# Performance work log

Hardware: AMD Instinct MI355X
Metric: run time of the kernel (lower is better)

The kernel has to match this reference:

```python
import jax, jax.numpy as jnp
import numpy as np

B, T, D, V, U = 16, 1000, 512, 5000, 64


def _safe_logaddexp(a, b):
    # logaddexp with nan-safe gradients when both args are -inf
    both = jnp.isneginf(a) & jnp.isneginf(b)
    a_ = jnp.where(both, 0.0, a)
    b_ = jnp.where(both, 0.0, b)
    return jnp.where(both, -jnp.inf, jnp.logaddexp(a_, b_))


def _log_sub_exp(a, b):
    # faithful port of log_substraction_exp: log(exp(a) - exp(b)), stable
    mask1 = (~jnp.isinf(a)) & (~jnp.isinf(b))
    a_ = jnp.where(mask1, a, -1.0)
    b_ = jnp.where(mask1, b, -2.0)
    ans_tmp = b_ + jnp.log(jnp.exp(a_ - b_) - 1.0)
    a_ = jnp.where(jnp.isinf(ans_tmp), -2000.0, a_)
    b_ = jnp.where(jnp.isinf(ans_tmp), -2001.0, b_)
    ans1 = b_ + jnp.log(jnp.exp(a_ - b_) - 1.0)
    ans = jnp.where(mask1, ans1, -jnp.inf)
    mask2 = (~jnp.isinf(a)) & jnp.isinf(b)
    return jnp.where(mask2, a, ans)


def _ctc_trellis(logp, ys):
    # Standard CTC lattice over extended labels (blank interleaved), S = 2U+1.
    # alpha[t,b,s]: logprob of paths over frames 0..t ending in state s (incl. emission at t)
    # beta[t,b,s]:  logprob of emitting frames t+1..T-1 and finishing, given state s at t
    # This reproduces the k2 lattice forward/backward scores at the label states.
    Bb, Tt, _ = logp.shape
    Uu = ys.shape[1]
    S = 2 * Uu + 1
    l_ext = jnp.zeros((Bb, S), ys.dtype).at[:, 1::2].set(ys)  # blank=0 at even s
    lp = jnp.take_along_axis(logp, jnp.broadcast_to(l_ext[:, None, :], (Bb, Tt, S)), axis=2)
    skip_ok = jnp.zeros((Bb, S), bool).at[:, 3::2].set(ys[:, 1:] != ys[:, :-1])
    lpT = jnp.transpose(lp, (1, 0, 2))  # [T,B,S]
    ninf1 = jnp.full((Bb, 1), -jnp.inf)
    ninf2 = jnp.full((Bb, 2), -jnp.inf)

    a0 = jnp.full((Bb, S), -jnp.inf).at[:, :2].set(lpT[0, :, :2])

    def astep(ap, lp_t):
        s1 = jnp.concatenate([ninf1, ap[:, :-1]], 1)
        s2 = jnp.concatenate([ninf2, ap[:, :-2]], 1)
        a = lp_t + _safe_logaddexp(_safe_logaddexp(ap, s1), jnp.where(skip_ok, s2, -jnp.inf))
        return a, a

    _, arest = jax.lax.scan(astep, a0, lpT[1:])
    alpha = jnp.concatenate([a0[None], arest], 0)  # [T,B,S]

    bl = jnp.full((Bb, S), -jnp.inf).at[:, S - 2:].set(0.0)  # final states: last label / last blank
    skipL2 = jnp.concatenate([skip_ok[:, 2:], jnp.zeros((Bb, 2), bool)], 1)

    def bstep(bn, lp_next):
        m = lp_next + bn
        m1 = jnp.concatenate([m[:, 1:], ninf1], 1)
        m2 = jnp.concatenate([m[:, 2:], ninf2], 1)
        bcur = _safe_logaddexp(_safe_logaddexp(m, m1), jnp.where(skipL2, m2, -jnp.inf))
        return bcur, bcur

    _, brest = jax.lax.scan(bstep, bl, lpT[1:], reverse=True)
    beta = jnp.concatenate([brest, bl[None]], 0)  # [T,B,S]
    return alpha, beta, lp


def setup_inputs() -> dict:
    key = jax.random.key(0)
    k1, k2, k3 = jax.random.split(key, 3)
    hs_pad = jax.random.normal(k1, (B, T, D), jnp.float32)
    hlens = jnp.full((B,), T, jnp.int32)
    ys_pad = jax.random.randint(k2, (B, U), 1, V)  # labels in [1, V); 0 is blank
    ali = jnp.zeros((B, U), jnp.int32)  # unused when risk_factor == 0
    W = jax.random.normal(k3, (D, V), jnp.float32) * 0.02
    b = jnp.zeros((V,), jnp.float32)
    return {"hs_pad": hs_pad, "hlens": hlens, "ys_pad": ys_pad, "ali": ali, "W": W, "b": b}


def reference(hs_pad, hlens, ys_pad, ali, W, b):
    # ctc_lo + log_softmax (dropout_rate=0). hlens are all equal -> sort/unsort is identity.
    logp = jax.nn.log_softmax(hs_pad @ W + b, axis=-1)  # [B,T,V]
    alpha_f, beta_f, lp = _ctc_trellis(logp, ys_pad)
    alpha = jnp.transpose(alpha_f[:, :, 1::2], (1, 2, 0))  # [B,U,T]
    beta = jnp.transpose(beta_f[:, :, 1::2], (1, 2, 0))    # [B,U,T]
    p = jnp.transpose(lp[:, :, 1::2], (0, 2, 1))           # [B,U,T] logprob of label u at frame t
    # beta', excluding re-emission of label u at t+1 -> paths whose label-u segment ends at t
    bp = _log_sub_exp(beta[:, :, :-1], beta[:, :, 1:] + p[:, :, 1:])
    bp = jnp.concatenate([bp, beta[:, :, -1:]], -1)
    loss_state = alpha + bp
    loss_state = jnp.where(jnp.isnan(loss_state), -jnp.inf, loss_state)
    loss_u = jax.nn.logsumexp(loss_state, axis=2)  # aggregate == 'time'
    mask = jnp.isinf(loss_u)
    denom = (~mask).astype(loss_u.dtype).sum(1)
    loss_fsas = jnp.where(mask, 0.0, loss_u).sum(1) / denom
    Uu = ys_pad.shape[1]
    loss_fsas = jnp.where(hlens < Uu, 0.0, loss_fsas)
    return (-loss_fsas).mean()
```

## Files before the change

### kernel.cpp

```cpp
#include <hip/hip_runtime.h>

#define NB 16
#define NT 1000
#define ND 512
#define NV 5000
#define NVP 5120
#define NU 64
#define NLL 72
#define NM (NB * NT)
#define NCH 40

typedef short short8v __attribute__((ext_vector_type(8)));
typedef float float4v __attribute__((ext_vector_type(4)));

#define NEGINF (-__builtin_inff())
#define SENTL  (-1.0e30f)
#define LOG2E 1.4426950408889634f
#define LN2F  0.6931471805599453f
#define SENT2 (-2000.4586751f * LOG2E)

__device__ __forceinline__ float fexp2(float x) { return __builtin_amdgcn_exp2f(x); }
__device__ __forceinline__ float flog2(float x) { return __builtin_amdgcn_logf(x); }

__device__ __forceinline__ float dpp_shr1(float x) {
  int xi = __builtin_bit_cast(int, x);
  int r = __builtin_amdgcn_update_dpp(xi, xi, 0x138, 0xf, 0xf, false);
  return __builtin_bit_cast(float, r);
}
__device__ __forceinline__ float dpp_shl1(float x) {
  int xi = __builtin_bit_cast(int, x);
  int r = __builtin_amdgcn_update_dpp(xi, xi, 0x130, 0xf, 0xf, false);
  return __builtin_bit_cast(float, r);
}

__device__ __forceinline__ short f2bf(float x) {
  unsigned int u = __builtin_bit_cast(unsigned int, x);
  unsigned int r = (u + 0x7fffu + ((u >> 16) & 1u)) >> 16;
  return (short)(unsigned short)r;
}
__device__ __forceinline__ float bf2f(short h) {
  unsigned int u = ((unsigned int)(unsigned short)h) << 16;
  return __builtin_bit_cast(float, u);
}

__device__ __forceinline__ void g2lds16(const short* g, short* l) {
  __builtin_amdgcn_global_load_lds(
      (const __attribute__((address_space(1))) void*)g,
      (__attribute__((address_space(3))) void*)l, 16, 0, 0);
}

__device__ __forceinline__ float lae2s(float a, float b) {
  float m = fmaxf(a, b);
  return m + flog2(fexp2(a - m) + fexp2(b - m));
}
__device__ __forceinline__ float lae3s(float a, float b, float c) {
  float m = fmaxf(fmaxf(a, b), c);
  return m + flog2(fexp2(a - m) + fexp2(b - m) + fexp2(c - m));
}
__device__ __forceinline__ float lsub2(float a, float b) {
  float tmp = b + flog2(fexp2(a - b) - 1.0f);
  if (__builtin_isinf(tmp)) tmp = SENT2;
  return tmp;
}

__global__ void k_zero(float* out) {
  if (threadIdx.x == 0) out[0] = 0.0f;
}

__global__ __launch_bounds__(256) void k_cvt_hs(const float* __restrict__ in,
                                                short* __restrict__ out) {
  size_t i = (size_t)blockIdx.x * 256 + threadIdx.x;
  const float4* p = (const float4*)in + i * 2;
  float4 v0 = p[0], v1 = p[1];
  short8v r;
  r[0] = f2bf(v0.x); r[1] = f2bf(v0.y); r[2] = f2bf(v0.z); r[3] = f2bf(v0.w);
  r[4] = f2bf(v1.x); r[5] = f2bf(v1.y); r[6] = f2bf(v1.z); r[7] = f2bf(v1.w);
  int row = (int)(i >> 6);
  int g = (int)(i & 63);
  int gs = (g & ~7) | ((g & 7) ^ (row & 7));
  *(short8v*)(out + (size_t)row * ND + gs * 8) = r;
}

__global__ __launch_bounds__(256) void k_cvt_wt(const float* __restrict__ W,
                                                short* __restrict__ WT,
                                                short* __restrict__ WTlo) {
  __shared__ short tileH[64 * 72];
  __shared__ short tileL[64 * 72];
  int n0 = blockIdx.x * 64, k0 = blockIdx.y * 64;
  int tid = threadIdx.x;
  int kr = tid >> 2, part = tid & 3;
  const float* src = W + (size_t)(k0 + kr) * NV + n0 + part * 16;
#pragma unroll
  for (int jj = 0; jj < 4; ++jj) {
    int c = n0 + part * 16 + jj * 4;
    float4 v;
    if (c + 3 < NV) {
      v = *(const float4*)(src + jj * 4);
    } else {
      v.x = (c + 0 < NV) ? src[jj * 4 + 0] : 0.f;
      v.y = (c + 1 < NV) ? src[jj * 4 + 1] : 0.f;
      v.z = (c + 2 < NV) ? src[jj * 4 + 2] : 0.f;
      v.w = (c + 3 < NV) ? src[jj * 4 + 3] : 0.f;
    }
    int base = kr * 72 + part * 16 + jj * 4;
    float vv[4] = {v.x, v.y, v.z, v.w};
#pragma unroll
    for (int q = 0; q < 4; ++q) {
      short h = f2bf(vv[q]);
      tileH[base + q] = h;
      tileL[base + q] = f2bf(vv[q] - bf2f(h));
    }
  }
  __syncthreads();
  int n = tid & 63, kq = tid >> 6;
  int nn = n0 + n;
  if (nn < NVP) {
#pragma unroll
    for (int half = 0; half < 2; ++half) {
      short8v vh, vl;
#pragma unroll
      for (int jj = 0; jj < 8; ++jj) {
        vh[jj] = tileH[(kq * 16 + half * 8 + jj) * 72 + n];
        vl[jj] = tileL[(kq * 16 + half * 8 + jj) * 72 + n];
      }
      int g = (k0 >> 3) + kq * 2 + half;
      int gs = (g & ~7) | ((g & 7) ^ (nn & 7));
      *(short8v*)(WT + (size_t)nn * ND + gs * 8) = vh;
      *(short8v*)(WTlo + (size_t)nn * ND + gs * 8) = vl;
    }
  }
}

__global__ __launch_bounds__(64) void k_gather2(const short* __restrict__ WT,
                                                const short* __restrict__ WTlo,
                                                const int* __restrict__ ys,
                                                short* __restrict__ Wg_hi,
                                                short* __restrict__ Wg_lo) {
  int u = blockIdx.x, b = blockIdx.y, t = threadIdx.x;
  short8v hi = {0,0,0,0,0,0,0,0}, lo = {0,0,0,0,0,0,0,0};
  if (u < NU + 1) {
    int lab = (u == 0) ? 0 : ys[b * NU + u - 1];
    int ps = (t & ~7) | ((t & 7) ^ (lab & 7));
    hi = *(const short8v*)(WT + (size_t)lab * ND + ps * 8);
    lo = *(const short8v*)(WTlo + (size_t)lab * ND + ps * 8);
  }
  int q = (t & ~7) | ((t & 7) ^ (u & 7));
  size_t base = ((size_t)(b * 128 + u)) * ND + q * 8;
  *(short8v*)(Wg_hi + base) = hi;
  *(short8v*)(Wg_lo + base) = lo;
}

__global__ __launch_bounds__(256) void k_labg(const short* __restrict__ hsb,
                                              const short* __restrict__ Wg_hi,
                                              const short* __restrict__ Wg_lo,
                                              const int* __restrict__ ys,
                                              const float* __restrict__ bias,
                                              float* __restrict__ ll) {
  __shared__ short As[128 * 64];
  __shared__ short Bh[128 * 64];
  __shared__ short Bl[128 * 64];

  int mt = blockIdx.x, b = blockIdx.y;
  int t0 = mt * 128;
  int tid = threadIdx.x;
  int lane = tid & 63, wave = tid >> 6;
  int wm = wave >> 1, wn = wave & 1;
  int lrow = lane & 15, lkhi = lane >> 4;

  const short* gaBase = hsb + (size_t)(b * NT + t0 + wave * 32 + (lane >> 3)) * ND + (lane & 7) * 8;
  const short* ghBase = Wg_hi + (size_t)(b * 128 + wave * 32 + (lane >> 3)) * ND + (lane & 7) * 8;
  const short* glBase = Wg_lo + (size_t)(b * 128 + wave * 32 + (lane >> 3)) * ND + (lane & 7) * 8;

  float4v acc[4][4];
#pragma unroll
  for (int m = 0; m < 4; ++m)
#pragma unroll
    for (int n = 0; n < 4; ++n)
#pragma unroll
      for (int j = 0; j < 4; ++j) acc[m][n][j] = 0.f;

  for (int s = 0; s < 8; ++s) {
    int k0 = s * 64;
#pragma unroll
    for (int i = 0; i < 4; ++i) {
      g2lds16(gaBase + (size_t)(i * 8) * ND + k0, &As[(wave * 32 + i * 8) * 64]);
      g2lds16(ghBase + (size_t)(i * 8) * ND + k0, &Bh[(wave * 32 + i * 8) * 64]);
      g2lds16(glBase + (size_t)(i * 8) * ND + k0, &Bl[(wave * 32 + i * 8) * 64]);
    }
    __syncthreads();
#pragma unroll
    for (int kk = 0; kk < 2; ++kk) {
      short8v av[4], bhv[4], blv2[4];
#pragma unroll
      for (int m = 0; m < 4; ++m) {
        int r = wm * 64 + m * 16 + lrow;
        int col = (kk * 32 + lkhi * 8) ^ ((r & 7) << 3);
        av[m] = *(const short8v*)&As[r * 64 + col];
      }
#pragma unroll
      for (int n = 0; n < 4; ++n) {
        int r = wn * 64 + n * 16 + lrow;
        int col = (kk * 32 + lkhi * 8) ^ ((r & 7) << 3);
        bhv[n] = *(const short8v*)&Bh[r * 64 + col];
        blv2[n] = *(const short8v*)&Bl[r * 64 + col];
      }
#pragma unroll
      for (int m = 0; m < 4; ++m)
#pragma unroll
        for (int n = 0; n < 4; ++n) {
          acc[m][n] = __builtin_amdgcn_mfma_f32_16x16x32_bf16(av[m], bhv[n], acc[m][n], 0, 0, 0);
          acc[m][n] = __builtin_amdgcn_mfma_f32_16x16x32_bf16(av[m], blv2[n], acc[m][n], 0, 0, 0);
        }
    }
    __syncthreads();
  }

  float bu[4]; bool uval[4];
#pragma unroll
  for (int n = 0; n < 4; ++n) {
    int u = wn * 64 + n * 16 + lrow;
    uval[n] = u < NU + 1;
    int lab = (u == 0) ? 0 : (uval[n] ? ys[b * NU + u - 1] : 0);
    bu[n] = uval[n] ? bias[lab] : 0.f;
  }
#pragma unroll
  for (int m = 0; m < 4; ++m)
#pragma unroll
    for (int j = 0; j < 4; ++j) {
      int trow = t0 + wm * 64 + m * 16 + lkhi * 4 + j;
      if (trow < NT) {
#pragma unroll
        for (int n = 0; n < 4; ++n) {
          int u = wn * 64 + n * 16 + lrow;
          if (uval[n])
            ll[((size_t)(b * NLL + u)) * NT + trow] = acc[m][n][j] + bu[n];
        }
      }
    }
}

__global__ __launch_bounds__(256) void k_denom(const short* __restrict__ hsb,
                                               const short* __restrict__ WT,
                                               const float* __restrict__ bias,
                                               float* __restrict__ pm,
                                               float* __restrict__ ps) {
  __shared__ short As[128 * 64];
  __shared__ short Ws[128 * 64];
  __shared__ float mred[128][2];
  __shared__ float sred[128][2];

  int lin = blockIdx.x;
  int o = (lin & 7) * 625 + (lin >> 3);
  int mt, chunk;
  if (o < 4800) {
    int sb = o / 320, w = o % 320;
    mt = sb * 8 + (w & 7);
    chunk = w >> 3;
  } else {
    int w = o - 4800;
    mt = 120 + (w % 5);
    chunk = w / 5;
  }
  int t0 = mt * 128;
  int n0 = chunk * 128;
  int tid = threadIdx.x;
  int lane = tid & 63, wave = tid >> 6;
  int wm = wave >> 1, wn = wave & 1;
  int lrow = lane & 15, lkhi = lane >> 4;

  const short* gaBase = hsb + (size_t)(t0 + wave * 32 + (lane >> 3)) * ND + (lane & 7) * 8;
  const short* gwBase = WT + (size_t)(n0 + wave * 32 + (lane >> 3)) * ND + (lane & 7) * 8;

  float4v acc[4][4];
#pragma unroll
  for (int m = 0; m < 4; ++m)
#pragma unroll
    for (int n = 0; n < 4; ++n)
#pragma unroll
      for (int j = 0; j < 4; ++j) acc[m][n][j] = 0.f;

  auto stage = [&](int s) {
    int k0 = s * 64;
#pragma unroll
    for (int i = 0; i < 4; ++i) {
      g2lds16(gaBase + (size_t)(i * 8) * ND + k0, &As[(wave * 32 + i * 8) * 64]);
      g2lds16(gwBase + (size_t)(i * 8) * ND + k0, &Ws[(wave * 32 + i * 8) * 64]);
    }
  };
  auto compute = [&]() {
#pragma unroll
    for (int kk = 0; kk < 2; ++kk) {
      short8v av[4], wv[4];
#pragma unroll
      for (int m = 0; m < 4; ++m) {
        int r = wm * 64 + m * 16 + lrow;
        int col = (kk * 32 + lkhi * 8) ^ ((r & 7) << 3);
        av[m] = *(const short8v*)&As[r * 64 + col];
      }
#pragma unroll
      for (int n = 0; n < 4; ++n) {
        int r = wn * 64 + n * 16 + lrow;
        int col = (kk * 32 + lkhi * 8) ^ ((r & 7) << 3);
        wv[n] = *(const short8v*)&Ws[r * 64 + col];
      }
#pragma unroll
      for (int m = 0; m < 4; ++m)
#pragma unroll
        for (int n = 0; n < 4; ++n)
          acc[m][n] = __builtin_amdgcn_mfma_f32_16x16x32_bf16(av[m], wv[n], acc[m][n], 0, 0, 0);
    }
  };

  for (int s = 0; s < 8; ++s) {
    stage(s);
    __syncthreads();
    compute();
    __syncthreads();
  }

  float bcol[4]; bool cval[4];
#pragma unroll
  for (int n = 0; n < 4; ++n) {
    int c = n0 + wn * 64 + n * 16 + lrow;
    cval[n] = c < NV;
    bcol[n] = cval[n] ? bias[c] : 0.f;
  }
#pragma unroll
  for (int m = 0; m < 4; ++m)
#pragma unroll
    for (int j = 0; j < 4; ++j) {
      float mx = NEGINF;
#pragma unroll
      for (int n = 0; n < 4; ++n) {
        float v = cval[n] ? acc[m][n][j] + bcol[n] : NEGINF;
        mx = fmaxf(mx, v);
      }
#pragma unroll
      for (int d = 1; d < 16; d <<= 1) mx = fmaxf(mx, __shfl_xor(mx, d));
      float mxc = fmaxf(mx, -3.0e38f);
      float p = 0.f;
#pragma unroll
      for (int n = 0; n < 4; ++n) {
        float v = cval[n] ? acc[m][n][j] + bcol[n] : NEGINF;
        p += __expf(v - mxc);
      }
#pragma unroll
      for (int d = 1; d < 16; d <<= 1) p += __shfl_xor(p, d);
      if (lrow == 0) {
        int rloc = wm * 64 + m * 16 + lkhi * 4 + j;
        mred[rloc][wn] = mx;
        sred[rloc][wn] = p;
      }
    }
  __syncthreads();
  if (tid < 128) {
    int row = t0 + tid;
    float m0 = mred[tid][0], m1 = mred[tid][1];
    float m = fmaxf(m0, m1);
    float ss = 0.f;
    if (m != NEGINF)
      ss = ((m0 == NEGINF) ? 0.f : sred[tid][0] * __expf(m0 - m))
         + ((m1 == NEGINF) ? 0.f : sred[tid][1] * __expf(m1 - m));
    pm[(size_t)chunk * NM + row] = m;
    ps[(size_t)chunk * NM + row] = ss;
  }
}

__global__ __launch_bounds__(256) void k_dred(const float* __restrict__ pm,
                                              const float* __restrict__ ps,
                                              float* __restrict__ denom) {
  int row = blockIdx.x * 256 + threadIdx.x;
  if (row >= NM) return;
  float m = NEGINF, s = 0.f;
  for (int c = 0; c < NCH; ++c) {
    float mc = pm[(size_t)c * NM + row];
    float sc = ps[(size_t)c * NM + row];
    if (mc == NEGINF) continue;
    if (mc > m) { s = s * __expf(m - mc) + sc; m = mc; }
    else        { s += sc * __expf(mc - m); }
  }
  denom[row] = m + __logf(s);
}

__global__ __launch_bounds__(64) void k_fwdbwd(const float* __restrict__ ll,
                                               const float* __restrict__ denom,
                                               const int* __restrict__ ys,
                                               float* __restrict__ aod,
                                               float* __restrict__ bp) {
  __shared__ float denS[NT];
  __shared__ float blkS[NT];
  int bid = blockIdx.x;
  int l = threadIdx.x;
  int b = (bid < NB) ? bid : bid - NB;
  const float* llb = ll + (size_t)b * NLL * NT;
  const float* denb = denom + b * NT;
#pragma unroll
  for (int i = 0; i < 16; ++i) {
    int idx = i * 64 + l;
    if (idx < NT) { denS[idx] = denb[idx]; blkS[idx] = llb[idx]; }
  }
  __syncthreads();
  const float* lrow = llb + (size_t)(1 + l) * NT;

  if (bid < NB) {
    int lab = ys[b * NU + l];
    int labp = ys[b * NU + ((l >= 1) ? (l - 1) : 0)];
    bool skip = (l >= 1) && (lab != labp);
    float* aodb = aod + (size_t)b * NT * NU;

    float den = denS[0];
    float ae = (l == 0) ? (blkS[0] - den) * LOG2E : SENTL;
    float ao = (l == 0) ? (lrow[0] - den) * LOG2E : SENTL;
    aodb[l] = ao;

    float cl[16];
#pragma unroll
    for (int j = 0; j < 16; ++j) {
      int tt = 1 + j; if (tt > NT - 1) tt = NT - 1;
      cl[j] = lrow[tt];
    }
    for (int g = 0; g < 63; ++g) {
      float nl[16];
      if (g < 62) {
#pragma unroll
        for (int j = 0; j < 16; ++j) {
          int tt = 17 + g * 16 + j; if (tt > NT - 1) tt = NT - 1;
          nl[j] = lrow[tt];
        }
      } else {
#pragma unroll
        for (int j = 0; j < 16; ++j) nl[j] = 0.f;
      }
#pragma unroll
      for (int j = 0; j < 16; ++j) {
        int t = 1 + g * 16 + j;
        if (t < NT) {
          float d2 = denS[t];
          float pb = (blkS[t] - d2) * LOG2E, pl = (cl[j] - d2) * LOG2E;
          float po = dpp_shr1(ao); if (l == 0) po = SENTL;
          float aen = pb + lae2s(ae, po);
          float aon = pl + lae3s(ao, ae, skip ? po : SENTL);
          ae = aen; ao = aon;
          aodb[t * NU + l] = ao;
        }
      }
#pragma unroll
      for (int j = 0; j < 16; ++j) cl[j] = nl[j];
    }
  } else {
    int lab = ys[b * NU + l];
    int labn = ys[b * NU + ((l < NU - 1) ? (l + 1) : l)];
    bool skipn = (l < NU - 1) && (labn != lab);
    float* bpb = bp + (size_t)b * NT * NU;

    float bo = (l == NU - 1) ? 0.0f : SENTL;
    float be = SENTL;
    float b128 = 0.0f;
    bpb[(NT - 1) * NU + l] = bo;

    float blv[16];
#pragma unroll
    for (int j = 0; j < 16; ++j) {
      int tt = NT - 2 - j; if (tt < 0) tt = 0;
      blv[j] = lrow[tt + 1];
    }
    for (int g = 0; g < 63; ++g) {
      float nl2[16];
      if (g < 62) {
#pragma unroll
        for (int j = 0; j < 16; ++j) {
          int tt = NT - 2 - 16 * (g + 1) - j; if (tt < 0) tt = 0;
          nl2[j] = lrow[tt + 1];
        }
      } else {
#pragma unroll
        for (int j = 0; j < 16; ++j) nl2[j] = 0.f;
      }
#pragma unroll
      for (int j = 0; j < 16; ++j) {
        int t = NT - 2 - 16 * g - j;
        if (t >= 0) {
          float d2 = denS[t + 1];
          float pbv = (blkS[t + 1] - d2) * LOG2E, plv = (blv[j] - d2) * LOG2E;
          float me = pbv + be;
          float mo = plv + bo;
          float m128 = pbv + b128;
          float ne = dpp_shl1(me); if (l == NU - 1) ne = m128;
          float no = dpp_shl1(mo); if (l == NU - 1) no = SENTL;
          float ben = lae2s(me, mo);
          float bon = lae3s(mo, ne, skipn ? no : SENTL);
          bpb[t * NU + l] = lsub2(bon, mo);
          be = ben; bo = bon; b128 = m128;
        }
      }
#pragma unroll
      for (int j = 0; j < 16; ++j) blv[j] = nl2[j];
    }
  }
}

__global__ __launch_bounds__(512) void k_loss(const float* __restrict__ aod,
                                              const float* __restrict__ bp,
                                              const int* __restrict__ hlens,
                                              float* __restrict__ out) {
  __shared__ float ms[8][64], ss[8][64];
  int b = blockIdx.x, tid = threadIdx.x;
  int w = tid >> 6, l = tid & 63;
  const float* ab = aod + (size_t)b * NT * NU;
  const float* pb = bp + (size_t)b * NT * NU;
  float m = NEGINF, s = 0.f;
  int t0 = w * 125, t1 = t0 + 125;
  for (int t = t0; t < t1; ++t) {
    float x = ab[t * NU + l] + pb[t * NU + l];
    if (__builtin_isnan(x) || x < -1.0e29f) continue;
    if (x > m) { s = s * fexp2(m - x) + 1.0f; m = x; }
    else       { s += fexp2(x - m); }
  }
  ms[w][l] = m; ss[w][l] = s;
  __syncthreads();
  if (w == 0) {
    float mm = NEGINF;
#pragma unroll
    for (int i = 0; i < 8; ++i) mm = fmaxf(mm, ms[i][l]);
    float lu;
    if (mm == NEGINF) lu = NEGINF;
    else {
      float st = 0.f;
#pragma unroll
      for (int i = 0; i < 8; ++i)
        st += (ms[i][l] == NEGINF) ? 0.f : ss[i][l] * fexp2(ms[i][l] - mm);
      lu = (mm + flog2(st)) * LN2F;
    }
    bool msk = __builtin_isinf(lu);
    float sv = msk ? 0.f : lu;
    float cv = msk ? 0.f : 1.f;
#pragma unroll
    for (int d = 1; d < 64; d <<= 1) { sv += __shfl_xor(sv, d); cv += __shfl_xor(cv, d); }
    if (l == 0) {
      float lf = sv / cv;
      if (hlens[b] < NU) lf = 0.f;
      atomicAdd(out, -lf * (1.0f / NB));
    }
  }
}

extern "C" void kernel_launch(void* const* d_in, const int* in_sizes, int n_in,
                              void* d_out, int out_size, void* d_ws, size_t ws_size,
                              hipStream_t stream) {
  const float* hs    = (const float*)d_in[0];
  const int*   hlens = (const int*)d_in[1];
  const int*   ys    = (const int*)d_in[2];
  const float* W     = (const float*)d_in[4];
  const float* bias  = (const float*)d_in[5];
  float* out = (float*)d_out;

  char* ws = (char*)d_ws;
  short* hsb   = (short*)(ws + 0);
  short* WT    = (short*)(ws + 16384000);
  short* WTlo  = (short*)(ws + 21626880);
  float* pm    = (float*)(ws + 26869760);
  float* psv   = (float*)(ws + 29429760);
  float* dnm   = (float*)(ws + 31989760);
  float* ll    = (float*)(ws + 32053760);
  short* Wg_hi = (short*)(ws + 26869760);
  short* Wg_lo = (short*)(ws + 28966912);
  float* aod   = (float*)(ws + 0);
  float* bpb   = (float*)(ws + 4096000);

  k_zero<<<1, 64, 0, stream>>>(out);
  k_cvt_hs<<<4000, 256, 0, stream>>>(hs, hsb);
  k_cvt_wt<<<dim3(80, 8), 256, 0, stream>>>(W, WT, WTlo);
  k_denom<<<5000, 256, 0, stream>>>(hsb, WT, bias, pm, psv);
  k_dred<<<63, 256, 0, stream>>>(pm, psv, dnm);
  k_gather2<<<dim3(128, 16), 64, 0, stream>>>(WT, WTlo, ys, Wg_hi, Wg_lo);
  k_labg<<<dim3(8, 16), 256, 0, stream>>>(hsb, Wg_hi, Wg_lo, ys, bias, ll);
  k_fwdbwd<<<32, 64, 0, stream>>>(ll, dnm, ys, aod, bpb);
  k_loss<<<16, 512, 0, stream>>>(aod, bpb, hlens, out);
}
```

Baseline: 365.6 us.

## Overlap CTC forward pass with denominator GEMM and fold normalizer into loss

The forward alpha recursion no longer needs the softmax denominator. It runs on unnormalized label logits inside the big denominator GEMM launch, as 16 extra blocks, so the serial recursion overlaps the GEMM. The per-frame log-normalizer is recomputed from per-chunk partials in the backward kernel, and its prefix sum is subtracted from alpha in the loss kernel. The zero, conversion and reduction kernels are merged, fewer padded label rows are gathered, and lsub2 gains an early exit. This removes several launches and the serial forward pass from the critical path, at the cost of redundant reductions and a risk of precision loss from large prefix sums.

```diff
diff --git a/kernel.cpp b/kernel.cpp
--- a/kernel.cpp
+++ b/kernel.cpp
@@ -6,7 +6,8 @@
 #define NV 5000
 #define NVP 5120
 #define NU 64
-#define NLL 72
+#define NLL 66
+#define NWG 72
 #define NM (NB * NT)
 #define NCH 40
 
@@ -58,35 +59,36 @@
   return m + flog2(fexp2(a - m) + fexp2(b - m) + fexp2(c - m));
 }
 __device__ __forceinline__ float lsub2(float a, float b) {
+  if (b < -1.0e29f) return (a < -1.0e29f) ? SENTL : a;
   float tmp = b + flog2(fexp2(a - b) - 1.0f);
   if (__builtin_isinf(tmp)) tmp = SENT2;
   return tmp;
 }
 
-__global__ void k_zero(float* out) {
-  if (threadIdx.x == 0) out[0] = 0.0f;
-}
-
-__global__ __launch_bounds__(256) void k_cvt_hs(const float* __restrict__ in,
-                                                short* __restrict__ out) {
-  size_t i = (size_t)blockIdx.x * 256 + threadIdx.x;
-  const float4* p = (const float4*)in + i * 2;
-  float4 v0 = p[0], v1 = p[1];
-  short8v r;
-  r[0] = f2bf(v0.x); r[1] = f2bf(v0.y); r[2] = f2bf(v0.z); r[3] = f2bf(v0.w);
-  r[4] = f2bf(v1.x); r[5] = f2bf(v1.y); r[6] = f2bf(v1.z); r[7] = f2bf(v1.w);
-  int row = (int)(i >> 6);
-  int g = (int)(i & 63);
-  int gs = (g & ~7) | ((g & 7) ^ (row & 7));
-  *(short8v*)(out + (size_t)row * ND + gs * 8) = r;
-}
-
-__global__ __launch_bounds__(256) void k_cvt_wt(const float* __restrict__ W,
-                                                short* __restrict__ WT,
-                                                short* __restrict__ WTlo) {
+__global__ __launch_bounds__(256) void k_cvt(const float* __restrict__ hs,
+                                             const float* __restrict__ W,
+                                             short* __restrict__ hsb,
+                                             short* __restrict__ WT,
+                                             short* __restrict__ WTlo,
+                                             float* __restrict__ outv) {
   __shared__ short tileH[64 * 72];
   __shared__ short tileL[64 * 72];
-  int n0 = blockIdx.x * 64, k0 = blockIdx.y * 64;
+  if (blockIdx.x < 4000) {
+    if (blockIdx.x == 0 && threadIdx.x == 0) outv[0] = 0.0f;
+    size_t i = (size_t)blockIdx.x * 256 + threadIdx.x;
+    const float4* p = (const float4*)hs + i * 2;
+    float4 v0 = p[0], v1 = p[1];
+    short8v r;
+    r[0] = f2bf(v0.x); r[1] = f2bf(v0.y); r[2] = f2bf(v0.z); r[3] = f2bf(v0.w);
+    r[4] = f2bf(v1.x); r[5] = f2bf(v1.y); r[6] = f2bf(v1.z); r[7] = f2bf(v1.w);
+    int row = (int)(i >> 6);
+    int g = (int)(i & 63);
+    int gs = (g & ~7) | ((g & 7) ^ (row & 7));
+    *(short8v*)(hsb + (size_t)row * ND + gs * 8) = r;
+    return;
+  }
+  int bx = blockIdx.x - 4000;
+  int n0 = (bx % 80) * 64, k0 = (bx / 80) * 64;
   int tid = threadIdx.x;
   int kr = tid >> 2, part = tid & 3;
   const float* src = W + (size_t)(k0 + kr) * NV + n0 + part * 16;
@@ -145,7 +147,7 @@
     lo = *(const short8v*)(WTlo + (size_t)lab * ND + ps * 8);
   }
   int q = (t & ~7) | ((t & 7) ^ (u & 7));
-  size_t base = ((size_t)(b * 128 + u)) * ND + q * 8;
+  size_t base = ((size_t)(b * NWG + u)) * ND + q * 8;
   *(short8v*)(Wg_hi + base) = hi;
   *(short8v*)(Wg_lo + base) = lo;
 }
@@ -168,8 +170,6 @@
   int lrow = lane & 15, lkhi = lane >> 4;
 
   const short* gaBase = hsb + (size_t)(b * NT + t0 + wave * 32 + (lane >> 3)) * ND + (lane & 7) * 8;
-  const short* ghBase = Wg_hi + (size_t)(b * 128 + wave * 32 + (lane >> 3)) * ND + (lane & 7) * 8;
-  const short* glBase = Wg_lo + (size_t)(b * 128 + wave * 32 + (lane >> 3)) * ND + (lane & 7) * 8;
 
   float4v acc[4][4];
 #pragma unroll
@@ -184,8 +184,12 @@
 #pragma unroll
     for (int i = 0; i < 4; ++i) {
       g2lds16(gaBase + (size_t)(i * 8) * ND + k0, &As[(wave * 32 + i * 8) * 64]);
-      g2lds16(ghBase + (size_t)(i * 8) * ND + k0, &Bh[(wave * 32 + i * 8) * 64]);
-      g2lds16(glBase + (size_t)(i * 8) * ND + k0, &Bl[(wave * 32 + i * 8) * 64]);
+      int brow = wave * 32 + (lane >> 3) + i * 8;
+      int brc = (brow < NWG - 1) ? brow : (NWG - 1);
+      g2lds16(Wg_hi + (size_t)(b * NWG + brc) * ND + (lane & 7) * 8 + k0,
+              &Bh[(wave * 32 + i * 8) * 64]);
+      g2lds16(Wg_lo + (size_t)(b * NWG + brc) * ND + (lane & 7) * 8 + k0,
+              &Bl[(wave * 32 + i * 8) * 64]);
     }
     __syncthreads();
 #pragma unroll
@@ -239,17 +243,77 @@
     }
 }
 
-__global__ __launch_bounds__(256) void k_denom(const short* __restrict__ hsb,
-                                               const short* __restrict__ WT,
-                                               const float* __restrict__ bias,
-                                               float* __restrict__ pm,
-                                               float* __restrict__ ps) {
+__global__ __launch_bounds__(256) void k_big(const short* __restrict__ hsb,
+                                             const short* __restrict__ WT,
+                                             const float* __restrict__ bias,
+                                             const float* __restrict__ ll,
+                                             const int* __restrict__ ys,
+                                             float* __restrict__ L,
+                                             float* __restrict__ aod) {
   __shared__ short As[128 * 64];
   __shared__ short Ws[128 * 64];
   __shared__ float mred[128][2];
   __shared__ float sred[128][2];
 
-  int lin = blockIdx.x;
+  int bid = blockIdx.x;
+  int tid = threadIdx.x;
+
+  if (bid < NB) {
+    float* blkS = (float*)As;
+    int b = bid;
+    const float* llb = ll + (size_t)b * NLL * NT;
+    for (int i = tid; i < NT; i += 256) blkS[i] = llb[i];
+    __syncthreads();
+    if (tid >= 64) return;
+    int l = tid;
+    const float* lrow = llb + (size_t)(1 + l) * NT;
+
+    int lab = ys[b * NU + l];
+    int labp = ys[b * NU + ((l >= 1) ? (l - 1) : 0)];
+    bool skip = (l >= 1) && (lab != labp);
+    float* aodb = aod + (size_t)b * NT * NU;
+
+    float ae = (l == 0) ? blkS[0] * LOG2E : SENTL;
+    float ao = (l == 0) ? lrow[0] * LOG2E : SENTL;
+    aodb[l] = ao;
+
+    float cl[16];
+#pragma unroll
+    for (int j = 0; j < 16; ++j) {
+      int tt = 1 + j; if (tt > NT - 1) tt = NT - 1;
+      cl[j] = lrow[tt];
+    }
+    for (int g = 0; g < 63; ++g) {
+      float nl[16];
+      if (g < 62) {
+#pragma unroll
+        for (int j = 0; j < 16; ++j) {
+          int tt = 17 + g * 16 + j; if (tt > NT - 1) tt = NT - 1;
+          nl[j] = lrow[tt];
+        }
+      } else {
+#pragma unroll
+        for (int j = 0; j < 16; ++j) nl[j] = 0.f;
+      }
+#pragma unroll
+      for (int j = 0; j < 16; ++j) {
+        int t = 1 + g * 16 + j;
+        if (t < NT) {
+          float pb = blkS[t] * LOG2E, pl = cl[j] * LOG2E;
+          float po = dpp_shr1(ao); if (l == 0) po = SENTL;
+          float aen = pb + lae2s(ae, po);
+          float aon = pl + lae3s(ao, ae, skip ? po : SENTL);
+          ae = aen; ao = aon;
+          aodb[t * NU + l] = ao;
+        }
+      }
+#pragma unroll
+      for (int j = 0; j < 16; ++j) cl[j] = nl[j];
+    }
+    return;
+  }
+
+  int lin = bid - NB;
   int o = (lin & 7) * 625 + (lin >> 3);
   int mt, chunk;
   if (o < 4800) {
@@ -263,7 +327,6 @@
   }
   int t0 = mt * 128;
   int n0 = chunk * 128;
-  int tid = threadIdx.x;
   int lane = tid & 63, wave = tid >> 6;
   int wm = wave >> 1, wn = wave & 1;
   int lrow = lane & 15, lkhi = lane >> 4;
@@ -279,15 +342,14 @@
 #pragma unroll
       for (int j = 0; j < 4; ++j) acc[m][n][j] = 0.f;
 
-  auto stage = [&](int s) {
+  for (int s = 0; s < 8; ++s) {
     int k0 = s * 64;
 #pragma unroll
     for (int i = 0; i < 4; ++i) {
       g2lds16(gaBase + (size_t)(i * 8) * ND + k0, &As[(wave * 32 + i * 8) * 64]);
       g2lds16(gwBase + (size_t)(i * 8) * ND + k0, &Ws[(wave * 32 + i * 8) * 64]);
     }
-  };
-  auto compute = [&]() {
+    __syncthreads();
 #pragma unroll
     for (int kk = 0; kk < 2; ++kk) {
       short8v av[4], wv[4];
@@ -309,12 +371,6 @@
         for (int n = 0; n < 4; ++n)
           acc[m][n] = __builtin_amdgcn_mfma_f32_16x16x32_bf16(av[m], wv[n], acc[m][n], 0, 0, 0);
     }
-  };
-
-  for (int s = 0; s < 8; ++s) {
-    stage(s);
-    __syncthreads();
-    compute();
     __syncthreads();
   }
 
@@ -361,157 +417,139 @@
     if (m != NEGINF)
       ss = ((m0 == NEGINF) ? 0.f : sred[tid][0] * __expf(m0 - m))
          + ((m1 == NEGINF) ? 0.f : sred[tid][1] * __expf(m1 - m));
-    pm[(size_t)chunk * NM + row] = m;
-    ps[(size_t)chunk * NM + row] = ss;
-  }
-}
-
-__global__ __launch_bounds__(256) void k_dred(const float* __restrict__ pm,
-                                              const float* __restrict__ ps,
-                                              float* __restrict__ denom) {
-  int row = blockIdx.x * 256 + threadIdx.x;
-  if (row >= NM) return;
-  float m = NEGINF, s = 0.f;
-  for (int c = 0; c < NCH; ++c) {
-    float mc = pm[(size_t)c * NM + row];
-    float sc = ps[(size_t)c * NM + row];
-    if (mc == NEGINF) continue;
-    if (mc > m) { s = s * __expf(m - mc) + sc; m = mc; }
-    else        { s += sc * __expf(mc - m); }
-  }
-  denom[row] = m + __logf(s);
-}
-
-__global__ __launch_bounds__(64) void k_fwdbwd(const float* __restrict__ ll,
-                                               const float* __restrict__ denom,
-                                               const int* __restrict__ ys,
-                                               float* __restrict__ aod,
-                                               float* __restrict__ bp) {
+    float Lv = (m == NEGINF || ss <= 0.f) ? NEGINF : m + __logf(ss);
+    L[(size_t)chunk * NM + row] = Lv;
+  }
+}
+
+__global__ __launch_bounds__(256) void k_bwd(const float* __restrict__ ll,
+                                             const float* __restrict__ L,
+                                             const int* __restrict__ ys,
+                                             float* __restrict__ bp) {
   __shared__ float denS[NT];
   __shared__ float blkS[NT];
-  int bid = blockIdx.x;
-  int l = threadIdx.x;
-  int b = (bid < NB) ? bid : bid - NB;
+  int b = blockIdx.x;
+  int tid = threadIdx.x;
   const float* llb = ll + (size_t)b * NLL * NT;
-  const float* denb = denom + b * NT;
-#pragma unroll
-  for (int i = 0; i < 16; ++i) {
-    int idx = i * 64 + l;
-    if (idx < NT) { denS[idx] = denb[idx]; blkS[idx] = llb[idx]; }
+  for (int t = tid; t < NT; t += 256) {
+    int row = b * NT + t;
+    float m40 = NEGINF;
+#pragma unroll 4
+    for (int c = 0; c < NCH; ++c) m40 = fmaxf(m40, L[(size_t)c * NM + row]);
+    float s = 0.f;
+#pragma unroll 4
+    for (int c = 0; c < NCH; ++c) {
+      float Lc = L[(size_t)c * NM + row];
+      if (Lc > -1.0e29f) s += __expf(Lc - m40);
+    }
+    denS[t] = m40 + __logf(s);
+    blkS[t] = llb[t];
   }
   __syncthreads();
+  if (tid >= 64) return;
+  int l = tid;
   const float* lrow = llb + (size_t)(1 + l) * NT;
 
-  if (bid < NB) {
-    int lab = ys[b * NU + l];
-    int labp = ys[b * NU + ((l >= 1) ? (l - 1) : 0)];
-    bool skip = (l >= 1) && (lab != labp);
-    float* aodb = aod + (size_t)b * NT * NU;
-
-    float den = denS[0];
-    float ae = (l == 0) ? (blkS[0] - den) * LOG2E : SENTL;
-    float ao = (l == 0) ? (lrow[0] - den) * LOG2E : SENTL;
-    aodb[l] = ao;
-
-    float cl[16];
+  int lab = ys[b * NU + l];
+  int labn = ys[b * NU + ((l < NU - 1) ? (l + 1) : l)];
+  bool skipn = (l < NU - 1) && (labn != lab);
+  float* bpb = bp + (size_t)b * NT * NU;
+
+  float bo = (l == NU - 1) ? 0.0f : SENTL;
+  float be = SENTL;
+  float b128 = 0.0f;
+  bpb[(NT - 1) * NU + l] = bo;
+
+  float blv[16];
+#pragma unroll
+  for (int j = 0; j < 16; ++j) {
+    int tt = NT - 2 - j; if (tt < 0) tt = 0;
+    blv[j] = lrow[tt + 1];
+  }
+  for (int g = 0; g < 63; ++g) {
+    float nl2[16];
+    if (g < 62) {
+#pragma unroll
+      for (int j = 0; j < 16; ++j) {
+        int tt = NT - 2 - 16 * (g + 1) - j; if (tt < 0) tt = 0;
+        nl2[j] = lrow[tt + 1];
+      }
+    } else {
+#pragma unroll
+      for (int j = 0; j < 16; ++j) nl2[j] = 0.f;
+    }
 #pragma unroll
     for (int j = 0; j < 16; ++j) {
-      int tt = 1 + j; if (tt > NT - 1) tt = NT - 1;
-      cl[j] = lrow[tt];
-    }
-    for (int g = 0; g < 63; ++g) {
-      float nl[16];
-      if (g < 62) {
-#pragma unroll
-        for (int j = 0; j < 16; ++j) {
-          int tt = 17 + g * 16 + j; if (tt > NT - 1) tt = NT - 1;
-          nl[j] = lrow[tt];
-        }
-      } else {
-#pragma unroll
-        for (int j = 0; j < 16; ++j) nl[j] = 0.f;
-      }
-#pragma unroll
-      for (int j = 0; j < 16; ++j) {
-        int t = 1 + g * 16 + j;
-        if (t < NT) {
-          float d2 = denS[t];
-          float pb = (blkS[t] - d2) * LOG2E, pl = (cl[j] - d2) * LOG2E;
-          float po = dpp_shr1(ao); if (l == 0) po = SENTL;
-          float aen = pb + lae2s(ae, po);
-          float aon = pl + lae3s(ao, ae, skip ? po : SENTL);
-          ae = aen; ao = aon;
-          aodb[t * NU + l] = ao;
-        }
-      }
-#pragma unroll
-      for (int j = 0; j < 16; ++j) cl[j] = nl[j];
-    }
-  } else {
-    int lab = ys[b * NU + l];
-    int labn = ys[b * NU + ((l < NU - 1) ? (l + 1) : l)];
-    bool skipn = (l < NU - 1) && (labn != lab);
-    float* bpb = bp + (size_t)b * NT * NU;
-
-    float bo = (l == NU - 1) ? 0.0f : SENTL;
-    float be = SENTL;
-    float b128 = 0.0f;
-    bpb[(NT - 1) * NU + l] = bo;
-
-    float blv[16];
-#pragma unroll
-    for (int j = 0; j < 16; ++j) {
-      int tt = NT - 2 - j; if (tt < 0) tt = 0;
-      blv[j] = lrow[tt + 1];
-    }
-    for (int g = 0; g < 63; ++g) {
-      float nl2[16];
-      if (g < 62) {
-#pragma unroll
-        for (int j = 0; j < 16; ++j) {
-          int tt = NT - 2 - 16 * (g + 1) - j; if (tt < 0) tt = 0;
-          nl2[j] = lrow[tt + 1];
-        }
-      } else {
-#pragma unroll
-        for (int j = 0; j < 16; ++j) nl2[j] = 0.f;
-      }
-#pragma unroll
-      for (int j = 0; j < 16; ++j) {
-        int t = NT - 2 - 16 * g - j;
-        if (t >= 0) {
-          float d2 = denS[t + 1];
-          float pbv = (blkS[t + 1] - d2) * LOG2E, plv = (blv[j] - d2) * LOG2E;
-          float me = pbv + be;
-          float mo = plv + bo;
-          float m128 = pbv + b128;
-          float ne = dpp_shl1(me); if (l == NU - 1) ne = m128;
-          float no = dpp_shl1(mo); if (l == NU - 1) no = SENTL;
-          float ben = lae2s(me, mo);
-          float bon = lae3s(mo, ne, skipn ? no : SENTL);
-          bpb[t * NU + l] = lsub2(bon, mo);
-          be = ben; bo = bon; b128 = m128;
-        }
-      }
-#pragma unroll
-      for (int j = 0; j < 16; ++j) blv[j] = nl2[j];
-    }
+      int t = NT - 2 - 16 * g - j;
+      if (t >= 0) {
+        float d2 = denS[t + 1];
+        float pbv = (blkS[t + 1] - d2) * LOG2E, plv = (blv[j] - d2) * LOG2E;
+        float me = pbv + be;
+        float mo = plv + bo;
+        float m128 = pbv + b128;
+        float ne = dpp_shl1(me); if (l == NU - 1) ne = m128;
+        float no = dpp_shl1(mo); if (l == NU - 1) no = SENTL;
+        float ben = lae2s(me, mo);
+        float bon = lae3s(mo, ne, skipn ? no : SENTL);
+        bpb[t * NU + l] = lsub2(bon, mo);
+        be = ben; bo = bon; b128 = m128;
+      }
+    }
+#pragma unroll
+    for (int j = 0; j < 16; ++j) blv[j] = nl2[j];
   }
 }
 
 __global__ __launch_bounds__(512) void k_loss(const float* __restrict__ aod,
                                               const float* __restrict__ bp,
+                                              const float* __restrict__ L,
                                               const int* __restrict__ hlens,
                                               float* __restrict__ out) {
+  __shared__ float denL[NT];
+  __shared__ float Dpre[NT];
+  __shared__ float choff[64];
   __shared__ float ms[8][64], ss[8][64];
   int b = blockIdx.x, tid = threadIdx.x;
+  for (int t = tid; t < NT; t += 512) {
+    int row = b * NT + t;
+    float m40 = NEGINF;
+#pragma unroll 4
+    for (int c = 0; c < NCH; ++c) m40 = fmaxf(m40, L[(size_t)c * NM + row]);
+    float s = 0.f;
+#pragma unroll 4
+    for (int c = 0; c < NCH; ++c) {
+      float Lc = L[(size_t)c * NM + row];
+      if (Lc > -1.0e29f) s += __expf(Lc - m40);
+    }
+    denL[t] = m40 + __logf(s);
+  }
+  __syncthreads();
+  if (tid < 64) {
+    float s = 0.f;
+#pragma unroll
+    for (int i = 0; i < 16; ++i) { int t = tid * 16 + i; if (t < NT) s += denL[t]; }
+    float v = s;
+#pragma unroll
+    for (int d = 1; d < 64; d <<= 1) { float u = __shfl_up(v, d); if (tid >= d) v += u; }
+    choff[tid] = v - s;
+  }
+  __syncthreads();
+  for (int t = tid; t < NT; t += 512) {
+    float s = choff[t >> 4];
+    int base = t & ~15;
+    for (int i = base; i <= t; ++i) s += denL[i];
+    Dpre[t] = s;
+  }
+  __syncthreads();
   int w = tid >> 6, l = tid & 63;
   const float* ab = aod + (size_t)b * NT * NU;
-  const float* pb = bp + (size_t)b * NT * NU;
+  const float* pbp = bp + (size_t)b * NT * NU;
   float m = NEGINF, s = 0.f;
   int t0 = w * 125, t1 = t0 + 125;
   for (int t = t0; t < t1; ++t) {
-    float x = ab[t * NU + l] + pb[t * NU + l];
+    float av = ab[t * NU + l];
+    float pv = pbp[t * NU + l];
+    float x = av - Dpre[t] * LOG2E + pv;
     if (__builtin_isnan(x) || x < -1.0e29f) continue;
     if (x > m) { s = s * fexp2(m - x) + 1.0f; m = x; }
     else       { s += fexp2(x - m); }
@@ -558,22 +596,17 @@
   short* hsb   = (short*)(ws + 0);
   short* WT    = (short*)(ws + 16384000);
   short* WTlo  = (short*)(ws + 21626880);
-  float* pm    = (float*)(ws + 26869760);
-  float* psv   = (float*)(ws + 29429760);
-  float* dnm   = (float*)(ws + 31989760);
-  float* ll    = (float*)(ws + 32053760);
-  short* Wg_hi = (short*)(ws + 26869760);
-  short* Wg_lo = (short*)(ws + 28966912);
-  float* aod   = (float*)(ws + 0);
-  float* bpb   = (float*)(ws + 4096000);
-
-  k_zero<<<1, 64, 0, stream>>>(out);
-  k_cvt_hs<<<4000, 256, 0, stream>>>(hs, hsb);
-  k_cvt_wt<<<dim3(80, 8), 256, 0, stream>>>(W, WT, WTlo);
-  k_denom<<<5000, 256, 0, stream>>>(hsb, WT, bias, pm, psv);
-  k_dred<<<63, 256, 0, stream>>>(pm, psv, dnm);
-  k_gather2<<<dim3(128, 16), 64, 0, stream>>>(WT, WTlo, ys, Wg_hi, Wg_lo);
+  float* ll    = (float*)(ws + 21626880);
+  float* L     = (float*)(ws + 25850880);
+  short* Wg_hi = (short*)(ws + 28410880);
+  short* Wg_lo = (short*)(ws + 29590528);
+  float* aod   = (float*)(ws + 28410880);
+  float* bpb   = (float*)(ws + 32506880);
+
+  k_cvt<<<4640, 256, 0, stream>>>(hs, W, hsb, WT, WTlo, out);
+  k_gather2<<<dim3(NWG, 16), 64, 0, stream>>>(WT, WTlo, ys, Wg_hi, Wg_lo);
   k_labg<<<dim3(8, 16), 256, 0, stream>>>(hsb, Wg_hi, Wg_lo, ys, bias, ll);
-  k_fwdbwd<<<32, 64, 0, stream>>>(ll, dnm, ys, aod, bpb);
-  k_loss<<<16, 512, 0, stream>>>(aod, bpb, hlens, out);
-}
+  k_big<<<5016, 256, 0, stream>>>(hsb, WT, bias, ll, ys, L, aod);
+  k_bwd<<<NB, 256, 0, stream>>>(ll, L, ys, bpb);
+  k_loss<<<16, 512, 0, stream>>>(aod, bpb, L, hlens, out);
+}
```

After: 429.1 us. 17.4% more time.
